# Performance work log

Hardware: AMD Instinct MI355X
Metric: run time of the kernel (lower is better)

## Reference

```python
import jax, jax.numpy as jnp
import numpy as np

NSIDE = 128
NLAT = 4 * NSIDE - 1          # 511 iso-latitude rings
NLON = 4 * NSIDE              # max pixels per ring (equatorial belt)
LMAX = NLAT                   # 511
MMAX = NLON // 2 + 1          # 257
NPIX = 12 * NSIDE * NSIDE     # 196608 HEALPix pixels (RING ordering)


def _healpix_geometry(nside, mmax):
    """Precompute per-ring synthesis tables for the irregular HEALPix iFFT.

    For ring k with nphi_k pixels and phase offset o_k, pixel longitudes are
    phi_{k,j} = 2*pi*(j + o_k)/nphi_k.  Real synthesis from one-sided spectrum:
        f_{k,j} = sum_m w_m * (Re(c_{k,m}) cos(m phi) - Im(c_{k,m}) sin(m phi)),
    w_0 = 1, w_m = 2 for m > 0 (irfft, norm='forward' convention as in
    torch-harmonics style SHT synthesis).  Returns dense [nlat, nlon, mmax]
    cos/sin tables masked to each ring's true length, plus the flat gather
    index mapping RING-ordered pixels into the padded [nlat, nlon] grid.
    """
    N = nside
    nlat, nlon = 4 * N - 1, 4 * N
    k = np.arange(nlat)
    # ring sizes: polar caps 4*i pixels, equatorial belt 4*N pixels
    nphi = np.where(k < N - 1, 4 * (k + 1),
                    np.where(k > 3 * N - 1, 4 * (4 * N - 1 - k), 4 * N))
    # phase offsets: caps shifted by half a pixel; belt alternates 1/2, 0
    off = np.where((k < N - 1) | (k > 3 * N - 1), 0.5,
                   np.where(((k - (N - 1)) % 2) == 0, 0.5, 0.0))
    j = np.arange(nlon)
    mask = (j[None, :] < nphi[:, None]).astype(np.float32)          # [nlat, nlon]
    phi = (2.0 * np.pi) * (j[None, :] + off[:, None]) / nphi[:, None]
    m = np.arange(mmax)
    w = np.where(m == 0, 1.0, 2.0).astype(np.float32)               # one-sided weights
    ang = (phi[:, :, None] * m[None, None, :]).astype(np.float32)   # [nlat, nlon, mmax]
    A = (w * np.cos(ang)) * mask[:, :, None]
    B = (-w * np.sin(ang)) * mask[:, :, None]
    # RING-ordered flat pixel -> (ring, j) -> padded-grid flat index
    starts = np.concatenate([[0], np.cumsum(nphi)[:-1]])
    ring = np.repeat(np.arange(nlat), nphi)
    jj = np.arange(int(nphi.sum())) - starts[ring]
    fidx = (ring * nlon + jj).astype(np.int32)
    return A.astype(np.float32), B.astype(np.float32), fidx


def setup_inputs() -> dict:
    key = jax.random.key(0)
    kx, kp = jax.random.split(key)
    # spectral coefficients, real view of complex [..., lmax, mmax]
    x = jax.random.normal(kx, (4, 16, LMAX, MMAX, 2), dtype=jnp.float32)
    # associated Legendre table buffer pct[m, l, k_ring] (random stand-in;
    # the real module precomputes normalized Legendre polynomials here)
    pct = jax.random.normal(kp, (MMAX, LMAX, NLAT), dtype=jnp.float32) * 0.05
    A, B, fidx = _healpix_geometry(NSIDE, MMAX)
    return {
        "x": x,
        "pct": pct,
        "A": jnp.asarray(A),
        "B": jnp.asarray(B),
        "fidx": jnp.asarray(fidx),
    }


def reference(x, pct, A, B, fidx):
    xr, xi = x[..., 0], x[..., 1]                       # [..., lmax, mmax]
    # Legendre contraction: '...lmn,mlk->...kmn' on the real view is simply
    # the same real contraction applied to Re and Im independently.
    Xr = jnp.einsum('...lm,mlk->...km', xr, pct)        # [..., nlat, mmax]
    Xi = jnp.einsum('...lm,mlk->...km', xi, pct)
    # irregular per-ring real iFFT synthesis on padded [nlat, nlon] grid
    grid = jnp.einsum('kjm,...km->...kj', A, Xr) + jnp.einsum('kjm,...km->...kj', B, Xi)
    flat = grid.reshape(grid.shape[:-2] + (NLAT * NLON,))
    return flat[..., fidx]                              # [..., npix] RING order
```

## Files before the change

### kernel.cpp

```cpp
#include <hip/hip_runtime.h>
#include <cstddef>

#define NSIDE_ 128
#define NLAT_  511
#define NLON_  512
#define LMAX_  511
#define MMAX_  257
#define NPIX_  196608
#define TWO_PI_ 6.28318530717958647692f

#define XELEMS_   16809856u
#define X2TELEMS_ 16842752u

typedef __attribute__((ext_vector_type(8))) short bf16x8;
typedef __attribute__((ext_vector_type(4))) float f32x4;

static __device__ __forceinline__ unsigned short f2bf(float f) {
    union { float f; unsigned int u; } v; v.f = f;
    unsigned int r = v.u + 0x7FFFu + ((v.u >> 16) & 1u);
    return (unsigned short)(r >> 16);
}

static __device__ __forceinline__ unsigned int cvtpk(float lo, float hi) {
    unsigned int d;
    asm("v_cvt_pk_bf16_f32 %0, %1, %2" : "=v"(d) : "v"(lo), "v"(hi));
    return d;
}

static __device__ __forceinline__ bf16x8 ld_pair(const unsigned int* p) {
    union { struct { uint2 a, b; } s; bf16x8 v; } t;
    t.s.a = *(const uint2*)p;
    t.s.b = *(const uint2*)(p + 2);
    return t.v;
}

__global__ __launch_bounds__(256) void pack_x_k(
    const float* __restrict__ x, unsigned short* __restrict__ x2T)
{
    __shared__ unsigned short lds[32][520];
    int b   = blockIdx.x;
    int l0  = blockIdx.y * 32;
    int tid = threadIdx.x;

    const float* src = x + ((size_t)b * LMAX_ + l0) * (2 * MMAX_);
    for (int li = 0; li < 32; ++li) {
        bool valid = (l0 + li) < LMAX_;
        for (int m2 = tid; m2 < 2 * MMAX_; m2 += 256) {
            float f = valid ? src[(size_t)li * (2 * MMAX_) + m2] : 0.f;
            lds[li][m2] = f2bf(f);
        }
    }
    __syncthreads();

    for (int m2 = tid; m2 < 2 * MMAX_; m2 += 256) {
        int m  = m2 >> 1;
        int rb = (m2 & 1) * 64 + b;
        unsigned short* dst = x2T + ((size_t)m * 128 + rb) * 512 + l0;
#pragma unroll
        for (int g = 0; g < 4; ++g) {
            unsigned int w0 = (unsigned int)lds[g*8+0][m2] | ((unsigned int)lds[g*8+1][m2] << 16);
            unsigned int w1 = (unsigned int)lds[g*8+2][m2] | ((unsigned int)lds[g*8+3][m2] << 16);
            unsigned int w2 = (unsigned int)lds[g*8+4][m2] | ((unsigned int)lds[g*8+5][m2] << 16);
            unsigned int w3 = (unsigned int)lds[g*8+6][m2] | ((unsigned int)lds[g*8+7][m2] << 16);
            *(uint4*)(dst + g * 8) = make_uint4(w0, w1, w2, w3);
        }
    }
}

__global__ __launch_bounds__(256, 3) void legendre5_k(
    const unsigned short* __restrict__ x2T,
    const float* __restrict__ pct,
    float* __restrict__ X)
{
    __shared__ __align__(16) unsigned int Apk[2][128 * 18];

    int bid = blockIdx.x;
    int xcd = bid & 7, n = bid >> 3;
    int kt = n & 3, mi = n >> 2;
    int m = mi * 8 + xcd;
    if (m >= MMAX_) return;

    int k0  = kt * 128;
    int tid = threadIdx.x;
    int lane = tid & 63, w = tid >> 6;
    int wk = (w >> 1) * 64, wrb = (w & 1) * 64;
    int r = lane & 15, g = lane >> 4;

    const float* pctm = pct + (size_t)m * (LMAX_ * NLAT_);
    const unsigned short* x2m = x2T + (size_t)m * (128 * 512);

    int kc = tid & 15;
    int lp = tid >> 4;
    int o7 = (k0 + kc + 112 <= NLAT_ - 1) ? 112 : (NLAT_ - 1 - (k0 + kc));

    f32x4 acc[4][4];
#pragma unroll
    for (int a = 0; a < 4; ++a)
#pragma unroll
        for (int c = 0; c < 4; ++c) acc[a][c] = (f32x4){0.f, 0.f, 0.f, 0.f};

    float e0[8], e1[8];
    bf16x8 Bfc[4], Bfn[4];

    {
        const float* pa = pctm + (size_t)(2 * lp)     * NLAT_ + k0 + kc;
        const float* pb = pctm + (size_t)(2 * lp + 1) * NLAT_ + k0 + kc;
#pragma unroll
        for (int i = 0; i < 7; ++i) { e0[i] = pa[16 * i]; e1[i] = pb[16 * i]; }
        e0[7] = pa[o7]; e1[7] = pb[o7];
#pragma unroll
        for (int rs = 0; rs < 4; ++rs)
            Bfc[rs] = *(const bf16x8*)(x2m + (size_t)(wrb + rs * 16 + r) * 512 + g * 8);
    }

#pragma unroll 2
    for (int s = 0; s < 16; ++s) {
        const int bsel = s & 1;
        unsigned int* wp = &Apk[bsel][0];
#pragma unroll
        for (int i = 0; i < 8; ++i) {
            unsigned int dwv = cvtpk(e0[i], e1[i]);
            int kk = kc + 16 * i;
            wp[kk * 18 + (lp ^ ((i & 3) << 2))] = dwv;
        }
        __syncthreads();

        if (s < 15) {
            int l0n = (s + 1) * 32;
            int la = l0n + 2 * lp, lb = la + 1;
            if (lb > LMAX_ - 1) lb = LMAX_ - 1;
            const float* pa = pctm + (size_t)la * NLAT_ + k0 + kc;
            const float* pb = pctm + (size_t)lb * NLAT_ + k0 + kc;
#pragma unroll
            for (int i = 0; i < 7; ++i) { e0[i] = pa[16 * i]; e1[i] = pb[16 * i]; }
            e0[7] = pa[o7]; e1[7] = pb[o7];
            int lbase = l0n + g * 8;
#pragma unroll
            for (int rs = 0; rs < 4; ++rs)
                Bfn[rs] = *(const bf16x8*)(x2m + (size_t)(wrb + rs * 16 + r) * 512 + lbase);
        }

        const unsigned int* rp = &Apk[bsel][0];
        bf16x8 Af[4];
#pragma unroll
        for (int ks = 0; ks < 4; ++ks) {
            int row = wk + ks * 16 + r;
            Af[ks] = ld_pair(rp + row * 18 + ((g * 4) ^ ((ks & 3) << 2)));
        }
#pragma unroll
        for (int ks = 0; ks < 4; ++ks)
#pragma unroll
            for (int rs = 0; rs < 4; ++rs)
                acc[ks][rs] = __builtin_amdgcn_mfma_f32_16x16x32_bf16(
                    Af[ks], Bfc[rs], acc[ks][rs], 0, 0, 0);

        if (s < 15) {
#pragma unroll
            for (int rs = 0; rs < 4; ++rs) Bfc[rs] = Bfn[rs];
        }
    }

    float wgt = (m == 0) ? 1.f : 2.f;
#pragma unroll
    for (int ks = 0; ks < 4; ++ks) {
#pragma unroll
        for (int rs = 0; rs < 4; ++rs) {
            int rb = wrb + rs * 16 + r;
#pragma unroll
            for (int i = 0; i < 4; ++i) {
                int k = k0 + wk + ks * 16 + g * 4 + i;
                if (k < NLAT_)
                    X[((size_t)k * MMAX_ + m) * 128 + rb] = acc[ks][rs][i] * wgt;
            }
        }
    }
}

__global__ __launch_bounds__(256, 3) void synth5_k(
    const float* __restrict__ X,
    float* __restrict__ out)
{
    __shared__ __align__(16) unsigned int Adw[2][256 * 18];
    __shared__ __align__(16) unsigned int Bdw[2][64 * 18];

    int k  = blockIdx.x;
    int jh = blockIdx.y;

    int nphi, start; float off;
    if (k < NSIDE_ - 1) {
        nphi  = 4 * (k + 1);
        start = 2 * k * (k + 1);
        off   = 0.5f;
    } else if (k <= 3 * NSIDE_ - 1) {
        nphi  = 4 * NSIDE_;
        start = 2 * (NSIDE_ - 1) * NSIDE_ + (k - (NSIDE_ - 1)) * 4 * NSIDE_;
        off   = (((k - (NSIDE_ - 1)) & 1) == 0) ? 0.5f : 0.f;
    } else {
        int t = NLAT_ - k;
        nphi  = 4 * t;
        start = NPIX_ - 2 * t * (t + 1);
        off   = 0.5f;
    }
    int jblk = jh * 256;
    if (jblk >= nphi) return;

    int tid  = threadIdx.x;
    int lane = tid & 63, w = tid >> 6;
    int r = lane & 15, g = lane >> 4;

    float theta = TWO_PI_ * ((float)(jblk + tid) + off) / (float)nphi;
    float dc, ds;
    sincosf(theta, &ds, &dc);
    float cs = 1.f, sn = 0.f;

    int bb = tid & 63, kq = tid >> 6;
    const float* Xk = X + (size_t)k * (MMAX_ * 128) + bb;

    int swzA = ((tid >> 4) & 3) << 2;
    int swzB = ((bb  >> 4) & 3) << 2;

    float bv[8];
#pragma unroll
    for (int i = 0; i < 8; ++i) {
        int kap = kq * 8 + i;
        bv[i] = Xk[(size_t)(kap >> 1) * 128 + (kap & 1) * 64];
    }
    unsigned int adw[16];
#pragma unroll
    for (int mi2 = 0; mi2 < 16; ++mi2) {
        adw[mi2] = cvtpk(cs, -sn);
        float cn = fmaf(cs, dc, -(sn * ds));
        float s2 = fmaf(sn, dc,  cs * ds);
        cs = cn; sn = s2;
    }
    unsigned int bdw[4];
#pragma unroll
    for (int q = 0; q < 4; ++q) bdw[q] = cvtpk(bv[2 * q], bv[2 * q + 1]);

    bool wact = (jblk + w * 64) < nphi;

    f32x4 acc[4][4];
#pragma unroll
    for (int a = 0; a < 4; ++a)
#pragma unroll
        for (int c = 0; c < 4; ++c) acc[a][c] = (f32x4){0.f, 0.f, 0.f, 0.f};

#pragma unroll 2
    for (int s = 0; s < 17; ++s) {
        const int bsel = s & 1;
        {
            unsigned int* ap = &Adw[bsel][tid * 18];
#pragma unroll
            for (int q = 0; q < 8; ++q)
                *(uint2*)(ap + ((2 * q) ^ swzA)) = make_uint2(adw[2 * q], adw[2 * q + 1]);
            unsigned int* bp = &Bdw[bsel][bb * 18];
            int cb = (kq * 4) ^ swzB;
            *(uint2*)(bp + cb)     = make_uint2(bdw[0], bdw[1]);
            *(uint2*)(bp + cb + 2) = make_uint2(bdw[2], bdw[3]);
        }
        __syncthreads();

        if (s < 16) {
            int kap0 = (s + 1) * 32 + kq * 8;
#pragma unroll
            for (int i = 0; i < 8; ++i) {
                int kap = kap0 + i;
                int mm  = kap >> 1;
                bv[i] = (mm < MMAX_) ? Xk[(size_t)mm * 128 + (kap & 1) * 64] : 0.f;
            }
        }
        if (s < 16) {
#pragma unroll
            for (int mi2 = 0; mi2 < 16; ++mi2) {
                adw[mi2] = cvtpk(cs, -sn);
                float cn = fmaf(cs, dc, -(sn * ds));
                float s2 = fmaf(sn, dc,  cs * ds);
                cs = cn; sn = s2;
            }
        }

        if (wact) {
            const unsigned int* arp = &Adw[bsel][0];
            const unsigned int* brp = &Bdw[bsel][0];
            bf16x8 Af[4], Bf[4];
#pragma unroll
            for (int ks = 0; ks < 4; ++ks) {
                int row = w * 64 + ks * 16 + r;
                Af[ks] = ld_pair(arp + row * 18 + ((g * 4) ^ ((ks & 3) << 2)));
            }
#pragma unroll
            for (int bs = 0; bs < 4; ++bs) {
                int row = bs * 16 + r;
                Bf[bs] = ld_pair(brp + row * 18 + ((g * 4) ^ ((bs & 3) << 2)));
            }
#pragma unroll
            for (int ks = 0; ks < 4; ++ks)
#pragma unroll
                for (int bs = 0; bs < 4; ++bs)
                    acc[ks][bs] = __builtin_amdgcn_mfma_f32_16x16x32_bf16(
                        Af[ks], Bf[bs], acc[ks][bs], 0, 0, 0);
        }

        if (s < 16) {
#pragma unroll
            for (int q = 0; q < 4; ++q) bdw[q] = cvtpk(bv[2 * q], bv[2 * q + 1]);
        }
    }

    if (wact) {
#pragma unroll
        for (int ks = 0; ks < 4; ++ks)
#pragma unroll
            for (int bs = 0; bs < 4; ++bs) {
                int b = bs * 16 + r;
#pragma unroll
                for (int i = 0; i < 4; ++i) {
                    int j = jblk + w * 64 + ks * 16 + g * 4 + i;
                    if (j < nphi)
                        out[(size_t)b * NPIX_ + start + j] = acc[ks][bs][i];
                }
            }
    }
}

__global__ __launch_bounds__(256) void legendre_k(
    const float* __restrict__ x,
    const float* __restrict__ pct,
    float* __restrict__ X)
{
    int k  = blockIdx.x * 256 + threadIdx.x;
    int m  = blockIdx.y;
    int bh = blockIdx.z;
    bool active = (k < NLAT_);
    if (!active) k = NLAT_ - 1;

    float accR[32], accI[32];
#pragma unroll
    for (int i = 0; i < 32; ++i) { accR[i] = 0.f; accI[i] = 0.f; }

    const float* pcol  = pct + (size_t)m * LMAX_ * NLAT_ + k;
    const float* xbase = x + (size_t)(bh * 32) * LMAX_ * MMAX_ * 2 + (size_t)m * 2;
    const size_t bstride = (size_t)LMAX_ * MMAX_ * 2;

    for (int l = 0; l < LMAX_; ++l) {
        float p = pcol[(size_t)l * NLAT_];
        const float* xl = xbase + (size_t)l * MMAX_ * 2;
#pragma unroll
        for (int bb = 0; bb < 32; ++bb) {
            accR[bb] = fmaf(xl[(size_t)bb * bstride],     p, accR[bb]);
            accI[bb] = fmaf(xl[(size_t)bb * bstride + 1], p, accI[bb]);
        }
    }
    if (active) {
        float wv = (m == 0) ? 1.f : 2.f;
        size_t base = ((size_t)k * MMAX_ + m) * 128 + bh * 32;
#pragma unroll
        for (int bb = 0; bb < 32; ++bb) {
            X[base + bb]      = accR[bb] * wv;
            X[base + 64 + bb] = accI[bb] * wv;
        }
    }
}

__global__ __launch_bounds__(256) void synth2_k(
    const float* __restrict__ X,
    float* __restrict__ out)
{
    int k  = blockIdx.x;
    int j  = blockIdx.y * 256 + threadIdx.x;
    int bh = blockIdx.z;

    int nphi, start; float off;
    if (k < NSIDE_ - 1) {
        nphi  = 4 * (k + 1);
        start = 2 * k * (k + 1);
        off   = 0.5f;
    } else if (k <= 3 * NSIDE_ - 1) {
        nphi  = 4 * NSIDE_;
        start = 2 * (NSIDE_ - 1) * NSIDE_ + (k - (NSIDE_ - 1)) * 4 * NSIDE_;
        off   = (((k - (NSIDE_ - 1)) & 1) == 0) ? 0.5f : 0.f;
    } else {
        int t = NLAT_ - k;
        nphi  = 4 * t;
        start = NPIX_ - 2 * t * (t + 1);
        off   = 0.5f;
    }
    if (blockIdx.y == 1 && nphi <= 256) return;
    bool store_ok = (j < nphi);

    float ang = TWO_PI_ * ((float)j + off) / (float)nphi;
    float dsn, dcs;
    sincosf(ang, &dsn, &dcs);

    const float* Xk = X + (size_t)k * MMAX_ * 128 + bh * 32;

    float acc[32];
#pragma unroll
    for (int i = 0; i < 32; ++i) acc[i] = 0.f;

    float c = 1.f, s = 0.f;
    for (int m = 0; m < MMAX_; ++m) {
        const float* xm = Xk + (size_t)m * 128;
#pragma unroll
        for (int bb = 0; bb < 32; ++bb) {
            acc[bb] = fmaf(c, xm[bb], acc[bb]);
            acc[bb] = fmaf(-s, xm[64 + bb], acc[bb]);
        }
        float cn = fmaf(c, dcs, -(s * dsn));
        float s2 = fmaf(s, dcs,  (c * dsn));
        c = cn; s = s2;
    }

    if (store_ok) {
        float* op = out + (size_t)(bh * 32) * NPIX_ + start + j;
#pragma unroll
        for (int bb = 0; bb < 32; ++bb)
            op[(size_t)bb * NPIX_] = acc[bb];
    }
}

extern "C" void kernel_launch(void* const* d_in, const int* in_sizes, int n_in,
                              void* d_out, int out_size, void* d_ws, size_t ws_size,
                              hipStream_t stream)
{
    const float* x   = (const float*)d_in[0];
    const float* pct = (const float*)d_in[1];
    float* out = (float*)d_out;
    float* X   = (float*)d_ws;

    size_t need = (size_t)XELEMS_ * 4 + (size_t)X2TELEMS_ * 2;
    if (ws_size >= need) {
        unsigned short* x2T = (unsigned short*)(X + XELEMS_);
        pack_x_k<<<dim3(64, 16), dim3(256), 0, stream>>>(x, x2T);
        legendre5_k<<<dim3(1056), dim3(256), 0, stream>>>(x2T, pct, X);
        synth5_k<<<dim3(NLAT_, 2), dim3(256), 0, stream>>>(X, out);
    } else {
        legendre_k<<<dim3(2, MMAX_, 2), dim3(256), 0, stream>>>(x, pct, X);
        synth2_k<<<dim3(NLAT_, 2, 2), dim3(256), 0, stream>>>(X, out);
    }
}
```

Before: 214.1 us.

## Precompute belt trig table, split belt/cap synthesis, deepen Legendre prefetch

```diff
diff --git a/kernel.cpp b/kernel.cpp
--- a/kernel.cpp
+++ b/kernel.cpp
@@ -11,6 +11,7 @@
 
 #define XELEMS_   16809856u
 #define X2TELEMS_ 16842752u
+#define TELEMS_   557056u
 
 typedef __attribute__((ext_vector_type(8))) short bf16x8;
 typedef __attribute__((ext_vector_type(4))) float f32x4;
@@ -25,6 +26,11 @@
     unsigned int d;
     asm("v_cvt_pk_bf16_f32 %0, %1, %2" : "=v"(d) : "v"(lo), "v"(hi));
     return d;
+}
+
+static __device__ __forceinline__ void bar_lds() {
+    asm volatile("s_waitcnt lgkmcnt(0)" ::: "memory");
+    __builtin_amdgcn_s_barrier();
 }
 
 static __device__ __forceinline__ bf16x8 ld_pair(const unsigned int* p) {
@@ -67,7 +73,25 @@
     }
 }
 
-__global__ __launch_bounds__(256, 3) void legendre5_k(
+__global__ __launch_bounds__(256) void trig_k(unsigned short* __restrict__ T)
+{
+    int id = blockIdx.x * 256 + threadIdx.x;
+    int p  = id >> 9, j = id & 511;
+    float off = p ? 0.f : 0.5f;
+    float theta = TWO_PI_ * ((float)j + off) / 512.f;
+    float dc, ds;
+    sincosf(theta, &ds, &dc);
+    float cs = 1.f, sn = 0.f;
+    unsigned int* row = (unsigned int*)(T + ((size_t)p * 512 + j) * 544);
+    for (int m = 0; m < 272; ++m) {
+        row[m] = (m < MMAX_) ? cvtpk(cs, -sn) : 0u;
+        float cn = fmaf(cs, dc, -(sn * ds));
+        float s2 = fmaf(sn, dc,  cs * ds);
+        cs = cn; sn = s2;
+    }
+}
+
+__global__ __launch_bounds__(256, 3) void legendre6_k(
     const unsigned short* __restrict__ x2T,
     const float* __restrict__ pct,
     float* __restrict__ X)
@@ -99,48 +123,45 @@
 #pragma unroll
         for (int c = 0; c < 4; ++c) acc[a][c] = (f32x4){0.f, 0.f, 0.f, 0.f};
 
-    float e0[8], e1[8];
+    float e0[2][8], e1[2][8];
     bf16x8 Bfc[4], Bfn[4];
 
-    {
-        const float* pa = pctm + (size_t)(2 * lp)     * NLAT_ + k0 + kc;
-        const float* pb = pctm + (size_t)(2 * lp + 1) * NLAT_ + k0 + kc;
-#pragma unroll
-        for (int i = 0; i < 7; ++i) { e0[i] = pa[16 * i]; e1[i] = pb[16 * i]; }
-        e0[7] = pa[o7]; e1[7] = pb[o7];
+    auto load_pct = [&](int step, float* a, float* b) {
+        int la = step * 32 + 2 * lp, lb2 = la + 1;
+        if (lb2 > LMAX_ - 1) lb2 = LMAX_ - 1;
+        const float* pa = pctm + (size_t)la  * NLAT_ + k0 + kc;
+        const float* pb = pctm + (size_t)lb2 * NLAT_ + k0 + kc;
+#pragma unroll
+        for (int i = 0; i < 7; ++i) { a[i] = pa[16 * i]; b[i] = pb[16 * i]; }
+        a[7] = pa[o7]; b[7] = pb[o7];
+    };
+    auto load_B = [&](int step, bf16x8* dst) {
+        int lbase = step * 32 + g * 8;
 #pragma unroll
         for (int rs = 0; rs < 4; ++rs)
-            Bfc[rs] = *(const bf16x8*)(x2m + (size_t)(wrb + rs * 16 + r) * 512 + g * 8);
-    }
-
-#pragma unroll 2
+            dst[rs] = *(const bf16x8*)(x2m + (size_t)(wrb + rs * 16 + r) * 512 + lbase);
+    };
+
+    load_pct(0, e0[0], e1[0]);
+    load_pct(1, e0[1], e1[1]);
+    load_B(0, Bfc);
+
+#pragma unroll
     for (int s = 0; s < 16; ++s) {
-        const int bsel = s & 1;
-        unsigned int* wp = &Apk[bsel][0];
+        const int p = s & 1;
+        unsigned int* wp = &Apk[p][0];
 #pragma unroll
         for (int i = 0; i < 8; ++i) {
-            unsigned int dwv = cvtpk(e0[i], e1[i]);
+            unsigned int dwv = cvtpk(e0[p][i], e1[p][i]);
             int kk = kc + 16 * i;
             wp[kk * 18 + (lp ^ ((i & 3) << 2))] = dwv;
         }
-        __syncthreads();
-
-        if (s < 15) {
-            int l0n = (s + 1) * 32;
-            int la = l0n + 2 * lp, lb = la + 1;
-            if (lb > LMAX_ - 1) lb = LMAX_ - 1;
-            const float* pa = pctm + (size_t)la * NLAT_ + k0 + kc;
-            const float* pb = pctm + (size_t)lb * NLAT_ + k0 + kc;
-#pragma unroll
-            for (int i = 0; i < 7; ++i) { e0[i] = pa[16 * i]; e1[i] = pb[16 * i]; }
-            e0[7] = pa[o7]; e1[7] = pb[o7];
-            int lbase = l0n + g * 8;
-#pragma unroll
-            for (int rs = 0; rs < 4; ++rs)
-                Bfn[rs] = *(const bf16x8*)(x2m + (size_t)(wrb + rs * 16 + r) * 512 + lbase);
-        }
-
-        const unsigned int* rp = &Apk[bsel][0];
+        bar_lds();
+
+        if (s < 14) load_pct(s + 2, e0[p], e1[p]);
+        if (s < 15) load_B(s + 1, Bfn);
+
+        const unsigned int* rp = &Apk[p][0];
         bf16x8 Af[4];
 #pragma unroll
         for (int ks = 0; ks < 4; ++ks) {
@@ -176,15 +197,292 @@
     }
 }
 
-__global__ __launch_bounds__(256, 3) void synth5_k(
+__global__ __launch_bounds__(256, 3) void synth_belt_k(
+    const float* __restrict__ X,
+    const unsigned short* __restrict__ T,
+    float* __restrict__ out)
+{
+    __shared__ __align__(16) unsigned int Bdw[2][64 * 18];
+
+    int k    = 127 + blockIdx.x;
+    int jblk = blockIdx.y * 256;
+    int start = 2 * (NSIDE_ - 1) * NSIDE_ + (k - (NSIDE_ - 1)) * 512;
+    int p = (k - 127) & 1;
+
+    int tid  = threadIdx.x;
+    int lane = tid & 63, w = tid >> 6;
+    int r = lane & 15, g = lane >> 4;
+
+    int bb = tid & 63, kq = tid >> 6;
+    const float* Xk = X + (size_t)k * (MMAX_ * 128) + bb;
+    const unsigned short* Tp = T + (size_t)p * (512 * 544);
+    int swzB = ((bb >> 4) & 3) << 2;
+
+    auto load_bv = [&](int step, float* bv) {
+        int kap0 = step * 32 + kq * 8;
+#pragma unroll
+        for (int i = 0; i < 8; ++i) {
+            int kap = kap0 + i, mm = kap >> 1;
+            bv[i] = (mm < MMAX_) ? Xk[(size_t)mm * 128 + (kap & 1) * 64] : 0.f;
+        }
+    };
+    auto load_A = [&](int step, bf16x8* dst) {
+        int cb = step * 32 + g * 8;
+#pragma unroll
+        for (int ks = 0; ks < 4; ++ks) {
+            int row = jblk + w * 64 + ks * 16 + r;
+            dst[ks] = *(const bf16x8*)(Tp + (size_t)row * 544 + cb);
+        }
+    };
+
+    float bv[8];
+    unsigned int bdw[4];
+    bf16x8 AfC[4], AfN[4];
+    load_bv(0, bv);
+    load_A(0, AfC);
+#pragma unroll
+    for (int q = 0; q < 4; ++q) bdw[q] = cvtpk(bv[2 * q], bv[2 * q + 1]);
+
+    f32x4 acc[4][4];
+#pragma unroll
+    for (int a = 0; a < 4; ++a)
+#pragma unroll
+        for (int c = 0; c < 4; ++c) acc[a][c] = (f32x4){0.f, 0.f, 0.f, 0.f};
+
+#pragma unroll 2
+    for (int s = 0; s < 17; ++s) {
+        const int bsel = s & 1;
+        {
+            unsigned int* bp = &Bdw[bsel][bb * 18];
+            int cb = (kq * 4) ^ swzB;
+            *(uint2*)(bp + cb)     = make_uint2(bdw[0], bdw[1]);
+            *(uint2*)(bp + cb + 2) = make_uint2(bdw[2], bdw[3]);
+        }
+        bar_lds();
+
+        if (s < 16) { load_bv(s + 1, bv); load_A(s + 1, AfN); }
+
+        const unsigned int* brp = &Bdw[bsel][0];
+        bf16x8 Bf[4];
+#pragma unroll
+        for (int bs = 0; bs < 4; ++bs) {
+            int row = bs * 16 + r;
+            Bf[bs] = ld_pair(brp + row * 18 + ((g * 4) ^ ((bs & 3) << 2)));
+        }
+#pragma unroll
+        for (int ks = 0; ks < 4; ++ks)
+#pragma unroll
+            for (int bs = 0; bs < 4; ++bs)
+                acc[ks][bs] = __builtin_amdgcn_mfma_f32_16x16x32_bf16(
+                    AfC[ks], Bf[bs], acc[ks][bs], 0, 0, 0);
+
+        if (s < 16) {
+#pragma unroll
+            for (int q = 0; q < 4; ++q) bdw[q] = cvtpk(bv[2 * q], bv[2 * q + 1]);
+#pragma unroll
+            for (int ks = 0; ks < 4; ++ks) AfC[ks] = AfN[ks];
+        }
+    }
+
+#pragma unroll
+    for (int ks = 0; ks < 4; ++ks)
+#pragma unroll
+        for (int bs = 0; bs < 4; ++bs) {
+            int b = bs * 16 + r;
+#pragma unroll
+            for (int i = 0; i < 4; ++i) {
+                int j = jblk + w * 64 + ks * 16 + g * 4 + i;
+                out[(size_t)b * NPIX_ + start + j] = acc[ks][bs][i];
+            }
+        }
+}
+
+__global__ __launch_bounds__(256, 3) void synth_caps_k(
     const float* __restrict__ X,
     float* __restrict__ out)
 {
     __shared__ __align__(16) unsigned int Adw[2][256 * 18];
     __shared__ __align__(16) unsigned int Bdw[2][64 * 18];
 
+    int cid = blockIdx.x;
+    int k  = (cid < 127) ? cid : (cid + 257);
+    int jh = blockIdx.y;
+
+    int nphi, start;
+    if (k < NSIDE_ - 1) {
+        nphi  = 4 * (k + 1);
+        start = 2 * k * (k + 1);
+    } else {
+        int t = NLAT_ - k;
+        nphi  = 4 * t;
+        start = NPIX_ - 2 * t * (t + 1);
+    }
+    float off = 0.5f;
+    int jblk = jh * 256;
+    if (jblk >= nphi) return;
+
+    int tid  = threadIdx.x;
+    int lane = tid & 63, w = tid >> 6;
+    int r = lane & 15, g = lane >> 4;
+
+    float theta = TWO_PI_ * ((float)(jblk + tid) + off) / (float)nphi;
+    float dc, ds;
+    sincosf(theta, &ds, &dc);
+    float cs = 1.f, sn = 0.f;
+
+    int bb = tid & 63, kq = tid >> 6;
+    const float* Xk = X + (size_t)k * (MMAX_ * 128) + bb;
+
+    int swzA = ((tid >> 4) & 3) << 2;
+    int swzB = ((bb  >> 4) & 3) << 2;
+
+    float bv[8];
+#pragma unroll
+    for (int i = 0; i < 8; ++i) {
+        int kap = kq * 8 + i;
+        bv[i] = Xk[(size_t)(kap >> 1) * 128 + (kap & 1) * 64];
+    }
+    unsigned int adw[16];
+#pragma unroll
+    for (int mi2 = 0; mi2 < 16; ++mi2) {
+        adw[mi2] = cvtpk(cs, -sn);
+        float cn = fmaf(cs, dc, -(sn * ds));
+        float s2 = fmaf(sn, dc,  cs * ds);
+        cs = cn; sn = s2;
+    }
+    unsigned int bdw[4];
+#pragma unroll
+    for (int q = 0; q < 4; ++q) bdw[q] = cvtpk(bv[2 * q], bv[2 * q + 1]);
+
+    bool wact = (jblk + w * 64) < nphi;
+
+    f32x4 acc[4][4];
+#pragma unroll
+    for (int a = 0; a < 4; ++a)
+#pragma unroll
+        for (int c = 0; c < 4; ++c) acc[a][c] = (f32x4){0.f, 0.f, 0.f, 0.f};
+
+#pragma unroll 2
+    for (int s = 0; s < 17; ++s) {
+        const int bsel = s & 1;
+        {
+            unsigned int* ap = &Adw[bsel][tid * 18];
+#pragma unroll
+            for (int q = 0; q < 8; ++q)
+                *(uint2*)(ap + ((2 * q) ^ swzA)) = make_uint2(adw[2 * q], adw[2 * q + 1]);
+            unsigned int* bp = &Bdw[bsel][bb * 18];
+            int cb = (kq * 4) ^ swzB;
+            *(uint2*)(bp + cb)     = make_uint2(bdw[0], bdw[1]);
+            *(uint2*)(bp + cb + 2) = make_uint2(bdw[2], bdw[3]);
+        }
+        bar_lds();
+
+        if (s < 16) {
+            int kap0 = (s + 1) * 32 + kq * 8;
+#pragma unroll
+            for (int i = 0; i < 8; ++i) {
+                int kap = kap0 + i, mm = kap >> 1;
+                bv[i] = (mm < MMAX_) ? Xk[(size_t)mm * 128 + (kap & 1) * 64] : 0.f;
+            }
+#pragma unroll
+            for (int mi2 = 0; mi2 < 16; ++mi2) {
+                adw[mi2] = cvtpk(cs, -sn);
+                float cn = fmaf(cs, dc, -(sn * ds));
+                float s2 = fmaf(sn, dc,  cs * ds);
+                cs = cn; sn = s2;
+            }
+        }
+
+        if (wact) {
+            const unsigned int* arp = &Adw[bsel][0];
+            const unsigned int* brp = &Bdw[bsel][0];
+            bf16x8 Af[4], Bf[4];
+#pragma unroll
+            for (int ks = 0; ks < 4; ++ks) {
+                int row = w * 64 + ks * 16 + r;
+                Af[ks] = ld_pair(arp + row * 18 + ((g * 4) ^ ((ks & 3) << 2)));
+            }
+#pragma unroll
+            for (int bs = 0; bs < 4; ++bs) {
+                int row = bs * 16 + r;
+                Bf[bs] = ld_pair(brp + row * 18 + ((g * 4) ^ ((bs & 3) << 2)));
+            }
+#pragma unroll
+            for (int ks = 0; ks < 4; ++ks)
+#pragma unroll
+                for (int bs = 0; bs < 4; ++bs)
+                    acc[ks][bs] = __builtin_amdgcn_mfma_f32_16x16x32_bf16(
+                        Af[ks], Bf[bs], acc[ks][bs], 0, 0, 0);
+        }
+
+        if (s < 16) {
+#pragma unroll
+            for (int q = 0; q < 4; ++q) bdw[q] = cvtpk(bv[2 * q], bv[2 * q + 1]);
+        }
+    }
+
+    if (wact) {
+#pragma unroll
+        for (int ks = 0; ks < 4; ++ks)
+#pragma unroll
+            for (int bs = 0; bs < 4; ++bs) {
+                int b = bs * 16 + r;
+#pragma unroll
+                for (int i = 0; i < 4; ++i) {
+                    int j = jblk + w * 64 + ks * 16 + g * 4 + i;
+                    if (j < nphi)
+                        out[(size_t)b * NPIX_ + start + j] = acc[ks][bs][i];
+                }
+            }
+    }
+}
+
+__global__ __launch_bounds__(256) void legendre_k(
+    const float* __restrict__ x,
+    const float* __restrict__ pct,
+    float* __restrict__ X)
+{
+    int k  = blockIdx.x * 256 + threadIdx.x;
+    int m  = blockIdx.y;
+    int bh = blockIdx.z;
+    bool active = (k < NLAT_);
+    if (!active) k = NLAT_ - 1;
+
+    float accR[32], accI[32];
+#pragma unroll
+    for (int i = 0; i < 32; ++i) { accR[i] = 0.f; accI[i] = 0.f; }
+
+    const float* pcol  = pct + (size_t)m * LMAX_ * NLAT_ + k;
+    const float* xbase = x + (size_t)(bh * 32) * LMAX_ * MMAX_ * 2 + (size_t)m * 2;
+    const size_t bstride = (size_t)LMAX_ * MMAX_ * 2;
+
+    for (int l = 0; l < LMAX_; ++l) {
+        float p = pcol[(size_t)l * NLAT_];
+        const float* xl = xbase + (size_t)l * MMAX_ * 2;
+#pragma unroll
+        for (int bb = 0; bb < 32; ++bb) {
+            accR[bb] = fmaf(xl[(size_t)bb * bstride],     p, accR[bb]);
+            accI[bb] = fmaf(xl[(size_t)bb * bstride + 1], p, accI[bb]);
+        }
+    }
+    if (active) {
+        float wv = (m == 0) ? 1.f : 2.f;
+        size_t base = ((size_t)k * MMAX_ + m) * 128 + bh * 32;
+#pragma unroll
+        for (int bb = 0; bb < 32; ++bb) {
+            X[base + bb]      = accR[bb] * wv;
+            X[base + 64 + bb] = accI[bb] * wv;
+        }
+    }
+}
+
+__global__ __launch_bounds__(256) void synth2_k(
+    const float* __restrict__ X,
+    float* __restrict__ out)
+{
     int k  = blockIdx.x;
-    int jh = blockIdx.y;
+    int j  = blockIdx.y * 256 + threadIdx.x;
+    int bh = blockIdx.z;
 
     int nphi, start; float off;
     if (k < NSIDE_ - 1) {
@@ -201,190 +499,6 @@
         start = NPIX_ - 2 * t * (t + 1);
         off   = 0.5f;
     }
-    int jblk = jh * 256;
-    if (jblk >= nphi) return;
-
-    int tid  = threadIdx.x;
-    int lane = tid & 63, w = tid >> 6;
-    int r = lane & 15, g = lane >> 4;
-
-    float theta = TWO_PI_ * ((float)(jblk + tid) + off) / (float)nphi;
-    float dc, ds;
-    sincosf(theta, &ds, &dc);
-    float cs = 1.f, sn = 0.f;
-
-    int bb = tid & 63, kq = tid >> 6;
-    const float* Xk = X + (size_t)k * (MMAX_ * 128) + bb;
-
-    int swzA = ((tid >> 4) & 3) << 2;
-    int swzB = ((bb  >> 4) & 3) << 2;
-
-    float bv[8];
-#pragma unroll
-    for (int i = 0; i < 8; ++i) {
-        int kap = kq * 8 + i;
-        bv[i] = Xk[(size_t)(kap >> 1) * 128 + (kap & 1) * 64];
-    }
-    unsigned int adw[16];
-#pragma unroll
-    for (int mi2 = 0; mi2 < 16; ++mi2) {
-        adw[mi2] = cvtpk(cs, -sn);
-        float cn = fmaf(cs, dc, -(sn * ds));
-        float s2 = fmaf(sn, dc,  cs * ds);
-        cs = cn; sn = s2;
-    }
-    unsigned int bdw[4];
-#pragma unroll
-    for (int q = 0; q < 4; ++q) bdw[q] = cvtpk(bv[2 * q], bv[2 * q + 1]);
-
-    bool wact = (jblk + w * 64) < nphi;
-
-    f32x4 acc[4][4];
-#pragma unroll
-    for (int a = 0; a < 4; ++a)
-#pragma unroll
-        for (int c = 0; c < 4; ++c) acc[a][c] = (f32x4){0.f, 0.f, 0.f, 0.f};
-
-#pragma unroll 2
-    for (int s = 0; s < 17; ++s) {
-        const int bsel = s & 1;
-        {
-            unsigned int* ap = &Adw[bsel][tid * 18];
-#pragma unroll
-            for (int q = 0; q < 8; ++q)
-                *(uint2*)(ap + ((2 * q) ^ swzA)) = make_uint2(adw[2 * q], adw[2 * q + 1]);
-            unsigned int* bp = &Bdw[bsel][bb * 18];
-            int cb = (kq * 4) ^ swzB;
-            *(uint2*)(bp + cb)     = make_uint2(bdw[0], bdw[1]);
-            *(uint2*)(bp + cb + 2) = make_uint2(bdw[2], bdw[3]);
-        }
-        __syncthreads();
-
-        if (s < 16) {
-            int kap0 = (s + 1) * 32 + kq * 8;
-#pragma unroll
-            for (int i = 0; i < 8; ++i) {
-                int kap = kap0 + i;
-                int mm  = kap >> 1;
-                bv[i] = (mm < MMAX_) ? Xk[(size_t)mm * 128 + (kap & 1) * 64] : 0.f;
-            }
-        }
-        if (s < 16) {
-#pragma unroll
-            for (int mi2 = 0; mi2 < 16; ++mi2) {
-                adw[mi2] = cvtpk(cs, -sn);
-                float cn = fmaf(cs, dc, -(sn * ds));
-                float s2 = fmaf(sn, dc,  cs * ds);
-                cs = cn; sn = s2;
-            }
-        }
-
-        if (wact) {
-            const unsigned int* arp = &Adw[bsel][0];
-            const unsigned int* brp = &Bdw[bsel][0];
-            bf16x8 Af[4], Bf[4];
-#pragma unroll
-            for (int ks = 0; ks < 4; ++ks) {
-                int row = w * 64 + ks * 16 + r;
-                Af[ks] = ld_pair(arp + row * 18 + ((g * 4) ^ ((ks & 3) << 2)));
-            }
-#pragma unroll
-            for (int bs = 0; bs < 4; ++bs) {
-                int row = bs * 16 + r;
-                Bf[bs] = ld_pair(brp + row * 18 + ((g * 4) ^ ((bs & 3) << 2)));
-            }
-#pragma unroll
-            for (int ks = 0; ks < 4; ++ks)
-#pragma unroll
-                for (int bs = 0; bs < 4; ++bs)
-                    acc[ks][bs] = __builtin_amdgcn_mfma_f32_16x16x32_bf16(
-                        Af[ks], Bf[bs], acc[ks][bs], 0, 0, 0);
-        }
-
-        if (s < 16) {
-#pragma unroll
-            for (int q = 0; q < 4; ++q) bdw[q] = cvtpk(bv[2 * q], bv[2 * q + 1]);
-        }
-    }
-
-    if (wact) {
-#pragma unroll
-        for (int ks = 0; ks < 4; ++ks)
-#pragma unroll
-            for (int bs = 0; bs < 4; ++bs) {
-                int b = bs * 16 + r;
-#pragma unroll
-                for (int i = 0; i < 4; ++i) {
-                    int j = jblk + w * 64 + ks * 16 + g * 4 + i;
-                    if (j < nphi)
-                        out[(size_t)b * NPIX_ + start + j] = acc[ks][bs][i];
-                }
-            }
-    }
-}
-
-__global__ __launch_bounds__(256) void legendre_k(
-    const float* __restrict__ x,
-    const float* __restrict__ pct,
-    float* __restrict__ X)
-{
-    int k  = blockIdx.x * 256 + threadIdx.x;
-    int m  = blockIdx.y;
-    int bh = blockIdx.z;
-    bool active = (k < NLAT_);
-    if (!active) k = NLAT_ - 1;
-
-    float accR[32], accI[32];
-#pragma unroll
-    for (int i = 0; i < 32; ++i) { accR[i] = 0.f; accI[i] = 0.f; }
-
-    const float* pcol  = pct + (size_t)m * LMAX_ * NLAT_ + k;
-    const float* xbase = x + (size_t)(bh * 32) * LMAX_ * MMAX_ * 2 + (size_t)m * 2;
-    const size_t bstride = (size_t)LMAX_ * MMAX_ * 2;
-
-    for (int l = 0; l < LMAX_; ++l) {
-        float p = pcol[(size_t)l * NLAT_];
-        const float* xl = xbase + (size_t)l * MMAX_ * 2;
-#pragma unroll
-        for (int bb = 0; bb < 32; ++bb) {
-            accR[bb] = fmaf(xl[(size_t)bb * bstride],     p, accR[bb]);
-            accI[bb] = fmaf(xl[(size_t)bb * bstride + 1], p, accI[bb]);
-        }
-    }
-    if (active) {
-        float wv = (m == 0) ? 1.f : 2.f;
-        size_t base = ((size_t)k * MMAX_ + m) * 128 + bh * 32;
-#pragma unroll
-        for (int bb = 0; bb < 32; ++bb) {
-            X[base + bb]      = accR[bb] * wv;
-            X[base + 64 + bb] = accI[bb] * wv;
-        }
-    }
-}
-
-__global__ __launch_bounds__(256) void synth2_k(
-    const float* __restrict__ X,
-    float* __restrict__ out)
-{
-    int k  = blockIdx.x;
-    int j  = blockIdx.y * 256 + threadIdx.x;
-    int bh = blockIdx.z;
-
-    int nphi, start; float off;
-    if (k < NSIDE_ - 1) {
-        nphi  = 4 * (k + 1);
-        start = 2 * k * (k + 1);
-        off   = 0.5f;
-    } else if (k <= 3 * NSIDE_ - 1) {
-        nphi  = 4 * NSIDE_;
-        start = 2 * (NSIDE_ - 1) * NSIDE_ + (k - (NSIDE_ - 1)) * 4 * NSIDE_;
-        off   = (((k - (NSIDE_ - 1)) & 1) == 0) ? 0.5f : 0.f;
-    } else {
-        int t = NLAT_ - k;
-        nphi  = 4 * t;
-        start = NPIX_ - 2 * t * (t + 1);
-        off   = 0.5f;
-    }
     if (blockIdx.y == 1 && nphi <= 256) return;
     bool store_ok = (j < nphi);
 
@@ -428,12 +542,15 @@
     float* out = (float*)d_out;
     float* X   = (float*)d_ws;
 
-    size_t need = (size_t)XELEMS_ * 4 + (size_t)X2TELEMS_ * 2;
+    size_t need = (size_t)XELEMS_ * 4 + (size_t)X2TELEMS_ * 2 + (size_t)TELEMS_ * 2;
     if (ws_size >= need) {
         unsigned short* x2T = (unsigned short*)(X + XELEMS_);
+        unsigned short* T   = x2T + X2TELEMS_;
+        trig_k<<<dim3(4), dim3(256), 0, stream>>>(T);
         pack_x_k<<<dim3(64, 16), dim3(256), 0, stream>>>(x, x2T);
-        legendre5_k<<<dim3(1056), dim3(256), 0, stream>>>(x2T, pct, X);
-        synth5_k<<<dim3(NLAT_, 2), dim3(256), 0, stream>>>(X, out);
+        legendre6_k<<<dim3(1056), dim3(256), 0, stream>>>(x2T, pct, X);
+        synth_belt_k<<<dim3(257, 2), dim3(256), 0, stream>>>(X, T, out);
+        synth_caps_k<<<dim3(254, 2), dim3(256), 0, stream>>>(X, out);
     } else {
         legendre_k<<<dim3(2, MMAX_, 2), dim3(256), 0, stream>>>(x, pct, X);
         synth2_k<<<dim3(NLAT_, 2, 2), dim3(256), 0, stream>>>(X, out);
```

New measurement: 266.3 us. 1.24x slower.
